# Kernel tuning notes

Hardware: AMD Instinct MI355X
Metric: run time of the kernel (lower is better)

The kernel has to match this reference:

```python
import jax, jax.numpy as jnp
import numpy as np

B, C, H, W = 8, 512, 64, 64
CH = C // 2          # channels per branch after chunk
R = CH // 4          # reduced channels (reduction=4)


def conv1x1(x, w, b):
    # x: [B,c,H,W], w: [o,c], b: [o]  (1x1 conv == per-pixel matmul)
    return jnp.einsum('oc,bchw->bohw', w, x) + b[None, :, None, None]


def spatial_self_corr(x, w1, b1, w2, b2, wo, bo):
    # DANet-style position attention. x: [B,CH,H,W]
    b_, c_, h_, w_ = x.shape
    n = h_ * w_
    q = conv1x1(x, w1, b1).reshape(b_, -1, n)   # [B,R,N]
    k = conv1x1(x, w2, b2).reshape(b_, -1, n)   # [B,R,N]
    attn = jax.nn.softmax(jnp.einsum('brn,brm->bnm', q, k), axis=-1)  # [B,N,N]
    out = jnp.einsum('brn,bnm->brm', k, attn)   # v = k (reduced channels), [B,R,N]
    out = out.reshape(b_, -1, h_, w_)
    return conv1x1(out, wo, bo)                 # [B,CH,H,W]


def channel_self_corr(x, wq, bq, wk, bk, wo, bo):
    # DANet-style channel attention over reduced channels. x: [B,CH,H,W]
    b_, c_, h_, w_ = x.shape
    n = h_ * w_
    q = conv1x1(x, wq, bq).reshape(b_, -1, n)   # [B,R,N]
    k = conv1x1(x, wk, bk).reshape(b_, -1, n)   # [B,R,N]
    attn = jax.nn.softmax(jnp.einsum('brn,bsn->brs', q, k), axis=-1)  # [B,R,R]
    out = jnp.einsum('brs,bsn->brn', attn, k)   # v = k (reduced channels)
    out = out.reshape(b_, -1, h_, w_)
    return conv1x1(out, wo, bo)                 # [B,CH,H,W]


def ckam_forward(top_feat, bottom_feat, wt, bt, wb, bb,
                 s_w1, s_b1, s_w2, s_b2, s_wo, s_bo,
                 c_wq, c_bq, c_wk, c_bk, c_wo, c_bo, f_w, f_b):
    top = conv1x1(top_feat, wt, bt)
    bottom = conv1x1(bottom_feat, wb, bb)
    x = top + bottom                            # [B,C,H,W]
    x1, x2 = jnp.split(x, 2, axis=1)            # each [B,C/2,H,W]
    ssc_out = spatial_self_corr(x1, s_w1, s_b1, s_w2, s_b2, s_wo, s_bo)
    csc_out = channel_self_corr(x2, c_wq, c_bq, c_wk, c_bk, c_wo, c_bo)
    out = jnp.concatenate([ssc_out, csc_out], axis=1)  # [B,C,H,W]
    return conv1x1(out, f_w, f_b)


def setup_inputs() -> dict:
    key = jax.random.key(0)
    ks = jax.random.split(key, 24)
    s = 0.02
    d = {
        'top_feat': jax.random.normal(ks[0], (B, C, H, W), jnp.float32),
        'bottom_feat': jax.random.normal(ks[1], (B, C, H, W), jnp.float32),
        'wt': jax.random.normal(ks[2], (C, C), jnp.float32) * s,
        'bt': jnp.zeros((C,), jnp.float32),
        'wb': jax.random.normal(ks[3], (C, C), jnp.float32) * s,
        'bb': jnp.zeros((C,), jnp.float32),
        's_w1': jax.random.normal(ks[4], (R, CH), jnp.float32) * s,
        's_b1': jnp.zeros((R,), jnp.float32),
        's_w2': jax.random.normal(ks[5], (R, CH), jnp.float32) * s,
        's_b2': jnp.zeros((R,), jnp.float32),
        's_wo': jax.random.normal(ks[6], (CH, R), jnp.float32) * s,
        's_bo': jnp.zeros((CH,), jnp.float32),
        'c_wq': jax.random.normal(ks[7], (R, CH), jnp.float32) * s,
        'c_bq': jnp.zeros((R,), jnp.float32),
        'c_wk': jax.random.normal(ks[8], (R, CH), jnp.float32) * s,
        'c_bk': jnp.zeros((R,), jnp.float32),
        'c_wo': jax.random.normal(ks[9], (CH, R), jnp.float32) * s,
        'c_bo': jnp.zeros((CH,), jnp.float32),
        'f_w': jax.random.normal(ks[10], (C, C), jnp.float32) * s,
        'f_b': jnp.zeros((C,), jnp.float32),
    }
    return d


def reference(top_feat, bottom_feat, wt, bt, wb, bb,
              s_w1, s_b1, s_w2, s_b2, s_wo, s_bo,
              c_wq, c_bq, c_wk, c_bk, c_wo, c_bo, f_w, f_b):
    return ckam_forward(top_feat, bottom_feat, wt, bt, wb, bb,
                        s_w1, s_b1, s_w2, s_b2, s_wo, s_bo,
                        c_wq, c_bq, c_wk, c_bk, c_wo, c_bo, f_w, f_b)
```

## Files before the change

kernel.cpp:

```cpp
#include <hip/hip_runtime.h>

typedef unsigned short u16;
typedef unsigned int   u32;
typedef __attribute__((ext_vector_type(8))) short short8;
typedef __attribute__((ext_vector_type(4))) float f32x4;

__device__ __forceinline__ u16 f2bf(float f) {
  u32 u = __float_as_uint(f);
  u32 r = u + 0x7fffu + ((u >> 16) & 1u);
  return (u16)(r >> 16);
}

__device__ __forceinline__ void gl_lds16(const u16* g, u16* l) {
  __builtin_amdgcn_global_load_lds(
      (const __attribute__((address_space(1))) u32*)g,
      (__attribute__((address_space(3))) u32*)l, 16, 0, 0);
}

__global__ __launch_bounds__(256) void k_combine_qk(
    const float* __restrict__ wt, const float* __restrict__ bt,
    const float* __restrict__ wb, const float* __restrict__ bb,
    const float* __restrict__ s_w1, const float* __restrict__ s_b1,
    const float* __restrict__ s_w2, const float* __restrict__ s_b2,
    const float* __restrict__ c_wq, const float* __restrict__ c_bq,
    const float* __restrict__ c_wk, const float* __restrict__ c_bk,
    u16* __restrict__ Wqkb, float* __restrict__ bqk) {
  int j = blockIdx.x;
  int g = j >> 6, r = j & 63;
  const float* sw; const float* sb;
  if (g == 0)      { sw = s_w1; sb = s_b1; }
  else if (g == 1) { sw = s_w2; sb = s_b2; }
  else if (g == 2) { sw = c_wq; sb = c_bq; }
  else             { sw = c_wk; sb = c_bk; }
  int cbase = (g < 2) ? 0 : 256;

  __shared__ float swr[256];
  __shared__ float red[256];
  int t = threadIdx.x;
  swr[t] = sw[r * 256 + t];
  __syncthreads();

  float a0 = 0.f, a1 = 0.f, a2 = 0.f, a3 = 0.f;
#pragma unroll 4
  for (int c = 0; c < 256; ++c) {
    float a = swr[c];
    int row = (cbase + c) * 512;
    a0 += a * wt[row + t];
    a1 += a * wt[row + 256 + t];
    a2 += a * wb[row + t];
    a3 += a * wb[row + 256 + t];
  }
  Wqkb[j * 1024 + t]       = f2bf(a0);
  Wqkb[j * 1024 + 256 + t] = f2bf(a1);
  Wqkb[j * 1024 + 512 + t] = f2bf(a2);
  Wqkb[j * 1024 + 768 + t] = f2bf(a3);

  red[t] = swr[t] * (bt[cbase + t] + bb[cbase + t]);
  __syncthreads();
  for (int s = 128; s > 0; s >>= 1) {
    if (t < s) red[t] += red[t + s];
    __syncthreads();
  }
  if (t == 0) bqk[j] = red[0] + sb[r];
}

__global__ __launch_bounds__(128) void k_combine_f(
    const float* __restrict__ f_w, const float* __restrict__ f_b,
    const float* __restrict__ s_wo, const float* __restrict__ s_bo,
    const float* __restrict__ c_wo, const float* __restrict__ c_bo,
    u16* __restrict__ Wfb, float* __restrict__ bfb) {
  int o = blockIdx.x;
  int t = threadIdx.x;
  __shared__ float fwr[512];
  __shared__ float red[128];
  for (int i = t; i < 512; i += 128) fwr[i] = f_w[o * 512 + i];
  __syncthreads();

  float acc = 0.f;
  if (t < 64) {
#pragma unroll 4
    for (int c = 0; c < 256; ++c) acc += fwr[c] * s_wo[c * 64 + t];
  } else {
    int rr = t - 64;
#pragma unroll 4
    for (int c = 0; c < 256; ++c) acc += fwr[256 + c] * c_wo[c * 64 + rr];
  }
  Wfb[o * 128 + t] = f2bf(acc);

  red[t] = fwr[t] * s_bo[t] + fwr[t + 128] * s_bo[t + 128]
         + fwr[256 + t] * c_bo[t] + fwr[384 + t] * c_bo[t + 128];
  __syncthreads();
  for (int s = 64; s > 0; s >>= 1) {
    if (t < s) red[t] += red[t + s];
    __syncthreads();
  }
  if (t == 0) bfb[o] = red[0] + f_b[o];
}

__global__ __launch_bounds__(256) void k_gemm_qk_mfma(
    const float* __restrict__ top, const float* __restrict__ bot,
    const u16* __restrict__ Wqkb, const float* __restrict__ bqk,
    float* __restrict__ qk) {
  int b = blockIdx.z, j0 = blockIdx.y * 128, n0 = blockIdx.x * 128;
  __shared__ __align__(16) u16 Aj[2][128][32];
  __shared__ __align__(16) u16 Xs[2][128][32];
  int t = threadIdx.x;
  int wv = t >> 6, lane = t & 63;
  int wr = wv >> 1, wc = wv & 1;
  int q = lane >> 4, l = lane & 15;

  f32x4 acc[4][4];
#pragma unroll
  for (int tr = 0; tr < 4; ++tr)
#pragma unroll
    for (int tc = 0; tc < 4; ++tc) acc[tr][tc] = (f32x4){0.f, 0.f, 0.f, 0.f};

  int xn = t & 31;
  int xs = t >> 5;
  int kx = (xn + (xn >> 2)) & 3;
  int wcol = ((((xs >> 1) ^ kx) << 4) | ((xs & 1) << 3));
  int asr4 = lane >> 2;
  int asc = (lane & 3) ^ ((asr4 + (asr4 >> 2)) & 3);
  int rowA = wr * 64 + l;
  int rowX = wc * 64 + l;
  int fswA = (q ^ ((rowA + (rowA >> 2)) & 3)) << 4;
  int fswX = (q ^ ((rowX + (rowX >> 2)) & 3)) << 4;

  float xva[16], xvb[16];

  auto stageA = [&](int kc, u16* dst) {
#pragma unroll
    for (int pp = 0; pp < 2; ++pp) {
      int p = wv * 2 + pp;
      int row = p * 16 + asr4;
      gl_lds16(Wqkb + (size_t)(j0 + row) * 1024 + kc + asc * 8, dst + p * 512);
    }
  };
  auto loadX = [&](int kc, float (&xv)[16]) {
    const float* src = (kc < 512) ? top : bot;
    int c0 = kc & 511;
    const float* xb = src + (size_t)(b * 512 + c0) * 4096 + n0;
#pragma unroll
    for (int p = 0; p < 4; ++p) {
      int n = xn + 32 * p;
#pragma unroll
      for (int d = 0; d < 4; ++d)
        xv[4 * p + d] = xb[(size_t)(4 * xs + d) * 4096 + n];
    }
  };
  auto writeX = [&](float (&xv)[16], u16* dst) {
    char* base = reinterpret_cast<char*>(dst);
#pragma unroll
    for (int p = 0; p < 4; ++p) {
      int n = xn + 32 * p;
      uint2 pk;
      pk.x = (u32)f2bf(xv[4 * p])     | ((u32)f2bf(xv[4 * p + 1]) << 16);
      pk.y = (u32)f2bf(xv[4 * p + 2]) | ((u32)f2bf(xv[4 * p + 3]) << 16);
      *reinterpret_cast<uint2*>(base + n * 64 + wcol) = pk;
    }
  };
  auto compute = [&](int bufsel) {
    const char* Ab = reinterpret_cast<const char*>(&Aj[bufsel][0][0]);
    const char* Xb = reinterpret_cast<const char*>(&Xs[bufsel][0][0]);
    short8 af[4], bfr[4];
#pragma unroll
    for (int tr = 0; tr < 4; ++tr)
      af[tr] = *reinterpret_cast<const short8*>(Ab + (rowA + tr * 16) * 64 + fswA);
#pragma unroll
    for (int tc = 0; tc < 4; ++tc)
      bfr[tc] = *reinterpret_cast<const short8*>(Xb + (rowX + tc * 16) * 64 + fswX);
#pragma unroll
    for (int tr = 0; tr < 4; ++tr)
#pragma unroll
      for (int tc = 0; tc < 4; ++tc)
        acc[tr][tc] = __builtin_amdgcn_mfma_f32_16x16x32_bf16(
            af[tr], bfr[tc], acc[tr][tc], 0, 0, 0);
  };

  loadX(0, xva);
  stageA(0, &Aj[0][0][0]);
  writeX(xva, &Xs[0][0][0]);
  loadX(32, xvb);
  __syncthreads();

  for (int it2 = 0; it2 < 15; ++it2) {
    int e = it2 * 2;
    loadX((e + 2) * 32, xva);
    stageA((e + 1) * 32, &Aj[1][0][0]);
    writeX(xvb, &Xs[1][0][0]);
    compute(0);
    __syncthreads();
    loadX((e + 3) * 32, xvb);
    stageA((e + 2) * 32, &Aj[0][0][0]);
    writeX(xva, &Xs[0][0][0]);
    compute(1);
    __syncthreads();
  }
  stageA(31 * 32, &Aj[1][0][0]);
  writeX(xvb, &Xs[1][0][0]);
  compute(0);
  __syncthreads();
  compute(1);

#pragma unroll
  for (int tr = 0; tr < 4; ++tr) {
    int j = j0 + wr * 64 + tr * 16 + q * 4;
    float4 bias = *reinterpret_cast<const float4*>(&bqk[j]);
#pragma unroll
    for (int tc = 0; tc < 4; ++tc) {
      int n = n0 + wc * 64 + tc * 16 + l;
      float* dst = qk + (size_t)(b * 256 + j) * 4096 + n;
      dst[0]        = acc[tr][tc][0] + bias.x;
      dst[4096]     = acc[tr][tc][1] + bias.y;
      dst[2 * 4096] = acc[tr][tc][2] + bias.z;
      dst[3 * 4096] = acc[tr][tc][3] + bias.w;
    }
  }
}

__global__ __launch_bounds__(256) void k_transpose_qk(
    const float* __restrict__ qk, u16* __restrict__ q1t, u16* __restrict__ k1t) {
  int b = blockIdx.y, n0 = blockIdx.x * 64;
  __shared__ u16 T[128][68];
  int t = threadIdx.x;
  for (int i = t; i < 8192; i += 256) {
    int j = i >> 6, n = i & 63;
    T[j][n] = f2bf(qk[((size_t)(b * 256) + j) * 4096 + n0 + n]);
  }
  __syncthreads();
  int n = t & 63, h = t >> 6;
  u16 buf[32];
#pragma unroll
  for (int jj = 0; jj < 32; ++jj) buf[jj] = T[h * 32 + jj][n];
  u16* dst;
  if (h < 2) dst = q1t + ((size_t)(b * 4096) + n0 + n) * 64 + h * 32;
  else       dst = k1t + ((size_t)(b * 4096) + n0 + n) * 64 + (h - 2) * 32;
  u32* d32 = reinterpret_cast<u32*>(dst);
#pragma unroll
  for (int k = 0; k < 16; ++k)
    d32[k] = (u32)buf[2 * k] | ((u32)buf[2 * k + 1] << 16);
}

__global__ __launch_bounds__(256) void k_sp_stats_mfma(
    const u16* __restrict__ q1t, const u16* __restrict__ k1t,
    float* __restrict__ dinv) {
  int b = blockIdx.y, n0 = blockIdx.x * 64;
  __shared__ u16 Qs[64][72];
  __shared__ float red[4][64][16];
  int t = threadIdx.x;
  int wv = t >> 6, lane = t & 63;
  int q = lane >> 4, l = lane & 15;

  {
    const u32* src = reinterpret_cast<const u32*>(q1t + ((size_t)(b * 4096) + n0) * 64);
    for (int i = t; i < 2048; i += 256) {
      int n = i >> 5, c = i & 31;
      reinterpret_cast<u32*>(&Qs[n][0])[c] = src[n * 32 + c];
    }
  }
  __syncthreads();

  short8 afr[4][2];
#pragma unroll
  for (int tn = 0; tn < 4; ++tn)
#pragma unroll
    for (int kh = 0; kh < 2; ++kh)
      afr[tn][kh] = *reinterpret_cast<const short8*>(&Qs[tn * 16 + l][kh * 32 + q * 8]);

  const u16* kbase = k1t + (size_t)b * 4096 * 64;
  float dsum[4][4];
#pragma unroll
  for (int tn = 0; tn < 4; ++tn)
#pragma unroll
    for (int i = 0; i < 4; ++i) dsum[tn][i] = 0.f;

  for (int mt = wv; mt < 64; mt += 4) {
    int m0 = mt * 64;
#pragma unroll
    for (int tm = 0; tm < 4; ++tm) {
      const u16* kp = kbase + ((size_t)(m0 + tm * 16 + l)) * 64;
      short8 b0 = *reinterpret_cast<const short8*>(kp + q * 8);
      short8 b1 = *reinterpret_cast<const short8*>(kp + 32 + q * 8);
#pragma unroll
      for (int tn = 0; tn < 4; ++tn) {
        f32x4 acc = {0.f, 0.f, 0.f, 0.f};
        acc = __builtin_amdgcn_mfma_f32_16x16x32_bf16(afr[tn][0], b0, acc, 0, 0, 0);
        acc = __builtin_amdgcn_mfma_f32_16x16x32_bf16(afr[tn][1], b1, acc, 0, 0, 0);
#pragma unroll
        for (int i = 0; i < 4; ++i) dsum[tn][i] += __expf(acc[i]);
      }
    }
  }

#pragma unroll
  for (int tn = 0; tn < 4; ++tn)
#pragma unroll
    for (int i = 0; i < 4; ++i)
      red[wv][tn * 16 + q * 4 + i][l] = dsum[tn][i];
  __syncthreads();
  if (t < 64) {
    float s = 0.f;
#pragma unroll
    for (int v = 0; v < 4; ++v)
#pragma unroll
      for (int u = 0; u < 16; ++u) s += red[v][t][u];
    dinv[(size_t)b * 4096 + n0 + t] = 1.0f / s;
  }
}

__global__ __launch_bounds__(256) void k_scale_k1d(
    const float* __restrict__ qk, const float* __restrict__ dinv,
    u16* __restrict__ k1d) {
  int b = blockIdx.x >> 6, r = blockIdx.x & 63;
  const float* src = qk + ((size_t)(b * 256) + 64 + r) * 4096;
  const float* dv = dinv + (size_t)b * 4096;
  u16* dst = k1d + ((size_t)(b * 64) + r) * 4096;
  for (int i = threadIdx.x; i < 4096; i += 256)
    dst[i] = f2bf(src[i] * dv[i]);
}

#define NSPLIT 2

__device__ __forceinline__ void stage_qk(const u16* qb, const u16* kb, int noff,
                                         u16* qdst, u16* kdst,
                                         int wv, int rsub, int scol) {
#pragma unroll
  for (int pp = 0; pp < 2; ++pp) {
    int p = wv * 2 + pp;
    int row = p * 8 + rsub;
    gl_lds16(qb + ((size_t)(noff + row)) * 64 + scol * 8, qdst + p * 512);
    gl_lds16(kb + (size_t)row * 4096 + noff + scol * 8, kdst + p * 512);
  }
}

__global__ __launch_bounds__(256) void k_sp_apply_mfma(
    const u16* __restrict__ q1t, const u16* __restrict__ k1t,
    const u16* __restrict__ k1d, float* __restrict__ spre) {
  int b = blockIdx.z, m0 = blockIdx.x * 64;
  int n_base = blockIdx.y * (4096 / NSPLIT);
  const int NT = 64 / NSPLIT;

  __shared__ __align__(16) u16 Qs[2][64][64];
  __shared__ __align__(16) u16 Ks[2][64][64];
  __shared__ __align__(16) u16 Wt[64][64];

  int t = threadIdx.x;
  int wv = t >> 6, lane = t & 63;
  int q = lane >> 4, l = lane & 15;
  int sw = l & 7;
  int rsub = lane >> 3;
  int scol = (lane & 7) ^ rsub;

  const u16* ktp = k1t + ((size_t)(b * 4096) + m0 + wv * 16 + l) * 64;
  short8 bS0 = *reinterpret_cast<const short8*>(ktp + q * 8);
  short8 bS1 = *reinterpret_cast<const short8*>(ktp + 32 + q * 8);

  const u16* qb = q1t + (size_t)b * 4096 * 64;
  const u16* kb = k1d + (size_t)b * 64 * 4096;

  f32x4 accO[4];
#pragma unroll
  for (int tr = 0; tr < 4; ++tr) accO[tr] = (f32x4){0.f, 0.f, 0.f, 0.f};

  stage_qk(qb, kb, n_base, &Qs[0][0][0], &Ks[0][0][0], wv, rsub, scol);
  __syncthreads();

  int wrow = wv * 16 + l;
  char* wp = reinterpret_cast<char*>(&Wt[wrow][0]);
  int c_a0 = (q ^ sw) << 4;
  int c_a1 = c_a0 ^ 64;

  int cur = 0;
  for (int nt = 0; nt < NT; ++nt) {
    if (nt + 1 < NT)
      stage_qk(qb, kb, n_base + (nt + 1) * 64,
               &Qs[cur ^ 1][0][0], &Ks[cur ^ 1][0][0], wv, rsub, scol);

    const u16(*Qc)[64] = Qs[cur];
    const u16(*Kc)[64] = Ks[cur];

#pragma unroll
    for (int tn = 0; tn < 4; ++tn) {
      const char* qrow = reinterpret_cast<const char*>(&Qc[tn * 16 + l][0]);
      short8 a0 = *reinterpret_cast<const short8*>(qrow + c_a0);
      short8 a1 = *reinterpret_cast<const short8*>(qrow + c_a1);
      f32x4 s = {0.f, 0.f, 0.f, 0.f};
      s = __builtin_amdgcn_mfma_f32_16x16x32_bf16(a0, bS0, s, 0, 0, 0);
      s = __builtin_amdgcn_mfma_f32_16x16x32_bf16(a1, bS1, s, 0, 0, 0);
      u16 w0 = f2bf(__expf(s[0]));
      u16 w1 = f2bf(__expf(s[1]));
      u16 w2 = f2bf(__expf(s[2]));
      u16 w3 = f2bf(__expf(s[3]));
      uint2 pk;
      pk.x = (u32)w0 | ((u32)w1 << 16);
      pk.y = (u32)w2 | ((u32)w3 << 16);
      *reinterpret_cast<uint2*>(
          wp + ((((tn * 2 + (q >> 1)) ^ sw) << 4) | ((q & 1) << 3))) = pk;
    }

    short8 bW0 = *reinterpret_cast<const short8*>(wp + c_a0);
    short8 bW1 = *reinterpret_cast<const short8*>(wp + c_a1);
#pragma unroll
    for (int tr = 0; tr < 4; ++tr) {
      const char* krow = reinterpret_cast<const char*>(&Kc[tr * 16 + l][0]);
      short8 a0 = *reinterpret_cast<const short8*>(krow + c_a0);
      short8 a1 = *reinterpret_cast<const short8*>(krow + c_a1);
      accO[tr] = __builtin_amdgcn_mfma_f32_16x16x32_bf16(a0, bW0, accO[tr], 0, 0, 0);
      accO[tr] = __builtin_amdgcn_mfma_f32_16x16x32_bf16(a1, bW1, accO[tr], 0, 0, 0);
    }

    __syncthreads();
    cur ^= 1;
  }

#pragma unroll
  for (int tr = 0; tr < 4; ++tr)
#pragma unroll
    for (int i = 0; i < 4; ++i)
      atomicAdd(&spre[(size_t)(b * 64 + tr * 16 + q * 4 + i) * 4096 + m0 + wrow],
                accO[tr][i]);
}

__global__ __launch_bounds__(256) void k_ch_scores(
    const float* __restrict__ qk, float* __restrict__ part) {
  int b = blockIdx.y, ch = blockIdx.x;
  const float* q2 = qk + (size_t)(b * 256 + 128) * 4096;
  const float* k2 = qk + (size_t)(b * 256 + 192) * 4096;
  __shared__ float Qs[64][65];
  __shared__ float Ks[64][65];
  int t = threadIdx.x, ti = t >> 4, tj = t & 15;
  float acc[4][4] = {};

  for (int sub = 0; sub < 2; ++sub) {
    int n0 = ch * 128 + sub * 64;
    __syncthreads();
    for (int i = t; i < 4096; i += 256) {
      int r = i >> 6, n = i & 63;
      Qs[r][n] = q2[(size_t)r * 4096 + n0 + n];
      Ks[r][n] = k2[(size_t)r * 4096 + n0 + n];
    }
    __syncthreads();
#pragma unroll
    for (int n = 0; n < 64; ++n) {
      float qa[4], ka[4];
#pragma unroll
      for (int i = 0; i < 4; ++i) qa[i] = Qs[ti * 4 + i][n];
#pragma unroll
      for (int jx = 0; jx < 4; ++jx) ka[jx] = Ks[tj * 4 + jx][n];
#pragma unroll
      for (int i = 0; i < 4; ++i)
#pragma unroll
        for (int jx = 0; jx < 4; ++jx) acc[i][jx] += qa[i] * ka[jx];
    }
  }
#pragma unroll
  for (int i = 0; i < 4; ++i)
#pragma unroll
    for (int jx = 0; jx < 4; ++jx)
      part[(size_t)(b * 32 + ch) * 4096 + (ti * 4 + i) * 64 + tj * 4 + jx] = acc[i][jx];
}

__global__ __launch_bounds__(64) void k_ch_softmax(
    const float* __restrict__ part, float* __restrict__ attn2) {
  int bid = blockIdx.x;
  int b = bid >> 6, r = bid & 63;
  int s = threadIdx.x;
  const float* p0 = part + (size_t)(b * 32) * 4096 + r * 64 + s;
  float sum = 0.f;
#pragma unroll
  for (int c = 0; c < 32; ++c) sum += p0[(size_t)c * 4096];
  float mx = sum;
#pragma unroll
  for (int o = 32; o > 0; o >>= 1) mx = fmaxf(mx, __shfl_xor(mx, o));
  float e = __expf(sum - mx);
  float den = e;
#pragma unroll
  for (int o = 32; o > 0; o >>= 1) den += __shfl_xor(den, o);
  attn2[(size_t)b * 4096 + r * 64 + s] = e / den;
}

__global__ __launch_bounds__(256) void k_ch_apply(
    const float* __restrict__ qk, const float* __restrict__ attn2,
    float* __restrict__ cpre) {
  int b = blockIdx.y;
  int t = threadIdx.x;
  int n = blockIdx.x * 64 + (t & 63);
  int qr = t >> 6;
  const float* k2 = qk + (size_t)(b * 256 + 192) * 4096;
  __shared__ float As[64][64];
  {
    float4* As4 = reinterpret_cast<float4*>(&As[0][0]);
    const float4* a4 = reinterpret_cast<const float4*>(attn2 + (size_t)b * 4096);
    for (int i = t; i < 1024; i += 256) As4[i] = a4[i];
  }
  __syncthreads();

  float acc[16];
#pragma unroll
  for (int rr = 0; rr < 16; ++rr) acc[rr] = 0.f;
  for (int s4 = 0; s4 < 64; s4 += 4) {
    float kv0 = k2[(size_t)(s4 + 0) * 4096 + n];
    float kv1 = k2[(size_t)(s4 + 1) * 4096 + n];
    float kv2 = k2[(size_t)(s4 + 2) * 4096 + n];
    float kv3 = k2[(size_t)(s4 + 3) * 4096 + n];
#pragma unroll
    for (int rr = 0; rr < 16; ++rr) {
      float4 w = *reinterpret_cast<const float4*>(&As[qr * 16 + rr][s4]);
      acc[rr] += w.x * kv0 + w.y * kv1 + w.z * kv2 + w.w * kv3;
    }
  }
#pragma unroll
  for (int rr = 0; rr < 16; ++rr)
    cpre[(size_t)(b * 64 + qr * 16 + rr) * 4096 + n] = acc[rr];
}

__global__ __launch_bounds__(256) void k_final_mfma(
    const float* __restrict__ spre, const float* __restrict__ cpre,
    const u16* __restrict__ Wfb, const float* __restrict__ bfb,
    float* __restrict__ out) {
  int b = blockIdx.z, o0 = blockIdx.y * 128, n0 = blockIdx.x * 128;
  __shared__ u16 Aj[128][40];
  __shared__ u16 Xs[128][40];
  int t = threadIdx.x;
  int wv = t >> 6, lane = t & 63;
  int wr = wv >> 1, wc = wv & 1;
  int q = lane >> 4, l = lane & 15;

  f32x4 acc[4][4];
#pragma unroll
  for (int tr = 0; tr < 4; ++tr)
#pragma unroll
    for (int tc = 0; tc < 4; ++tc) acc[tr][tc] = (f32x4){0.f, 0.f, 0.f, 0.f};

  int xn = t & 31;
  int xs = t >> 5;

  for (int kc = 0; kc < 128; kc += 32) {
    __syncthreads();
    {
      const u32* asrc = reinterpret_cast<const u32*>(Wfb + (size_t)o0 * 128 + kc);
#pragma unroll
      for (int p = 0; p < 8; ++p) {
        int i = p * 256 + t;
        int row = i >> 4, c = i & 15;
        *reinterpret_cast<u32*>(&Aj[row][c * 2]) = asrc[(size_t)row * 64 + c];
      }
    }
    const float* src = (kc < 64) ? spre : cpre;
    int r0 = (kc < 64) ? kc : kc - 64;
    const float* xb = src + (size_t)(b * 64 + r0) * 4096 + n0;
#pragma unroll
    for (int p = 0; p < 8; ++p) {
      int n = xn + 32 * (p >> 1);
      int kp = xs + 8 * (p & 1);
      float v0 = xb[(size_t)(2 * kp) * 4096 + n];
      float v1 = xb[(size_t)(2 * kp + 1) * 4096 + n];
      *reinterpret_cast<u32*>(&Xs[n][kp * 2]) =
          (u32)f2bf(v0) | ((u32)f2bf(v1) << 16);
    }
    __syncthreads();

    short8 af[4], bfr[4];
#pragma unroll
    for (int tr = 0; tr < 4; ++tr)
      af[tr] = *reinterpret_cast<const short8*>(&Aj[wr * 64 + tr * 16 + l][q * 8]);
#pragma unroll
    for (int tc = 0; tc < 4; ++tc)
      bfr[tc] = *reinterpret_cast<const short8*>(&Xs[wc * 64 + tc * 16 + l][q * 8]);
#pragma unroll
    for (int tr = 0; tr < 4; ++tr)
#pragma unroll
      for (int tc = 0; tc < 4; ++tc)
        acc[tr][tc] = __builtin_amdgcn_mfma_f32_16x16x32_bf16(
            af[tr], bfr[tc], acc[tr][tc], 0, 0, 0);
  }

#pragma unroll
  for (int tr = 0; tr < 4; ++tr) {
    int o = o0 + wr * 64 + tr * 16 + q * 4;
    float4 bias = *reinterpret_cast<const float4*>(&bfb[o]);
#pragma unroll
    for (int tc = 0; tc < 4; ++tc) {
      int n = n0 + wc * 64 + tc * 16 + l;
      float* dst = out + (size_t)(b * 512 + o) * 4096 + n;
      dst[0]        = acc[tr][tc][0] + bias.x;
      dst[4096]     = acc[tr][tc][1] + bias.y;
      dst[2 * 4096] = acc[tr][tc][2] + bias.z;
      dst[3 * 4096] = acc[tr][tc][3] + bias.w;
    }
  }
}

extern "C" void kernel_launch(void* const* d_in, const int* in_sizes, int n_in,
                              void* d_out, int out_size, void* d_ws, size_t ws_size,
                              hipStream_t stream) {
  const float* top  = (const float*)d_in[0];
  const float* bot  = (const float*)d_in[1];
  const float* wt   = (const float*)d_in[2];
  const float* bt   = (const float*)d_in[3];
  const float* wb   = (const float*)d_in[4];
  const float* bb   = (const float*)d_in[5];
  const float* s_w1 = (const float*)d_in[6];
  const float* s_b1 = (const float*)d_in[7];
  const float* s_w2 = (const float*)d_in[8];
  const float* s_b2 = (const float*)d_in[9];
  const float* s_wo = (const float*)d_in[10];
  const float* s_bo = (const float*)d_in[11];
  const float* c_wq = (const float*)d_in[12];
  const float* c_bq = (const float*)d_in[13];
  const float* c_wk = (const float*)d_in[14];
  const float* c_bk = (const float*)d_in[15];
  const float* c_wo = (const float*)d_in[16];
  const float* c_bo = (const float*)d_in[17];
  const float* f_w  = (const float*)d_in[18];
  const float* f_b  = (const float*)d_in[19];
  float* out = (float*)d_out;

  char* ob = (char*)d_out;
  float* qk = (float*)ob;
  u16* q1t = (u16*)(ob + 33554432);
  u16* k1t = (u16*)(ob + 37748736);
  u16* k1d = (u16*)(ob + 41943040);
  float* part = (float*)(ob + 46137344);

  char* ws = (char*)d_ws;
  float* dinv  = (float*)(ws + 0);
  float* attn2 = (float*)(ws + 1179648);
  float* spre  = (float*)(ws + 1310720);
  float* cpre  = (float*)(ws + 9699328);
  u16*   Wqkb  = (u16*)  (ws + 18087936);
  float* bqk   = (float*)(ws + 18612224);
  u16*   Wfb   = (u16*)  (ws + 18613248);
  float* bfb   = (float*)(ws + 18744320);

  hipMemsetAsync(spre, 0, 8388608, stream);

  k_combine_qk<<<256, 256, 0, stream>>>(wt, bt, wb, bb, s_w1, s_b1, s_w2, s_b2,
                                        c_wq, c_bq, c_wk, c_bk, Wqkb, bqk);
  k_combine_f<<<512, 128, 0, stream>>>(f_w, f_b, s_wo, s_bo, c_wo, c_bo, Wfb, bfb);
  k_gemm_qk_mfma<<<dim3(32, 2, 8), 256, 0, stream>>>(top, bot, Wqkb, bqk, qk);
  k_transpose_qk<<<dim3(64, 8), 256, 0, stream>>>(qk, q1t, k1t);
  k_sp_stats_mfma<<<dim3(64, 8), 256, 0, stream>>>(q1t, k1t, dinv);
  k_ch_scores<<<dim3(32, 8), 256, 0, stream>>>(qk, part);
  k_ch_softmax<<<512, 64, 0, stream>>>(part, attn2);
  k_ch_apply<<<dim3(64, 8), 256, 0, stream>>>(qk, attn2, cpre);
  k_scale_k1d<<<512, 256, 0, stream>>>(qk, dinv, k1d);
  k_sp_apply_mfma<<<dim3(64, NSPLIT, 8), 256, 0, stream>>>(q1t, k1t, k1d, spre);
  k_final_mfma<<<dim3(32, 4, 8), 256, 0, stream>>>(spre, cpre, Wfb, bfb, out);
}
```

Before: 436.4 us.

## Shrink QK GEMM tile to 64 rows with swizzled grid and fuse k1d scaling into stats

The QK projection GEMM now uses 64x128 output tiles over a flat 1024-block grid whose block index is remapped so that the four j-tiles sharing an X tile run close together. The aim is more blocks in flight on the many CUs and better L2 reuse of the fp32 input. The cost is that each block reloads and converts X for a smaller slice of outputs. Separately, the row-normaliser scaling of k1 is folded into the softmax-stats kernel, which removes one launch and the dinv round trip through global memory.

```diff
diff --git a/kernel.cpp b/kernel.cpp
--- a/kernel.cpp
+++ b/kernel.cpp
@@ -101,19 +101,24 @@
     const float* __restrict__ top, const float* __restrict__ bot,
     const u16* __restrict__ Wqkb, const float* __restrict__ bqk,
     float* __restrict__ qk) {
-  int b = blockIdx.z, j0 = blockIdx.y * 128, n0 = blockIdx.x * 128;
-  __shared__ __align__(16) u16 Aj[2][128][32];
+  int bid = blockIdx.x;
+  int jt = (bid >> 3) & 3;
+  int idx = (bid >> 5) * 8 + (bid & 7);
+  int j0 = jt * 64;
+  int n0 = (idx & 31) * 128;
+  int b  = idx >> 5;
+
+  __shared__ __align__(16) u16 Aj[2][64][32];
   __shared__ __align__(16) u16 Xs[2][128][32];
   int t = threadIdx.x;
   int wv = t >> 6, lane = t & 63;
-  int wr = wv >> 1, wc = wv & 1;
   int q = lane >> 4, l = lane & 15;
 
-  f32x4 acc[4][4];
+  f32x4 acc[4][2];
 #pragma unroll
   for (int tr = 0; tr < 4; ++tr)
 #pragma unroll
-    for (int tc = 0; tc < 4; ++tc) acc[tr][tc] = (f32x4){0.f, 0.f, 0.f, 0.f};
+    for (int tc = 0; tc < 2; ++tc) acc[tr][tc] = (f32x4){0.f, 0.f, 0.f, 0.f};
 
   int xn = t & 31;
   int xs = t >> 5;
@@ -121,20 +126,13 @@
   int wcol = ((((xs >> 1) ^ kx) << 4) | ((xs & 1) << 3));
   int asr4 = lane >> 2;
   int asc = (lane & 3) ^ ((asr4 + (asr4 >> 2)) & 3);
-  int rowA = wr * 64 + l;
-  int rowX = wc * 64 + l;
-  int fswA = (q ^ ((rowA + (rowA >> 2)) & 3)) << 4;
-  int fswX = (q ^ ((rowX + (rowX >> 2)) & 3)) << 4;
+  int fsw = (q ^ ((l + (l >> 2)) & 3)) << 4;
 
   float xva[16], xvb[16];
 
   auto stageA = [&](int kc, u16* dst) {
-#pragma unroll
-    for (int pp = 0; pp < 2; ++pp) {
-      int p = wv * 2 + pp;
-      int row = p * 16 + asr4;
-      gl_lds16(Wqkb + (size_t)(j0 + row) * 1024 + kc + asc * 8, dst + p * 512);
-    }
+    int row = wv * 16 + asr4;
+    gl_lds16(Wqkb + (size_t)(j0 + row) * 1024 + kc + asc * 8, dst + wv * 512);
   };
   auto loadX = [&](int kc, float (&xv)[16]) {
     const float* src = (kc < 512) ? top : bot;
@@ -162,17 +160,18 @@
   auto compute = [&](int bufsel) {
     const char* Ab = reinterpret_cast<const char*>(&Aj[bufsel][0][0]);
     const char* Xb = reinterpret_cast<const char*>(&Xs[bufsel][0][0]);
-    short8 af[4], bfr[4];
+    short8 af[4], bfr[2];
 #pragma unroll
     for (int tr = 0; tr < 4; ++tr)
-      af[tr] = *reinterpret_cast<const short8*>(Ab + (rowA + tr * 16) * 64 + fswA);
-#pragma unroll
-    for (int tc = 0; tc < 4; ++tc)
-      bfr[tc] = *reinterpret_cast<const short8*>(Xb + (rowX + tc * 16) * 64 + fswX);
+      af[tr] = *reinterpret_cast<const short8*>(Ab + (tr * 16 + l) * 64 + fsw);
+#pragma unroll
+    for (int tc = 0; tc < 2; ++tc)
+      bfr[tc] = *reinterpret_cast<const short8*>(
+          Xb + (wv * 32 + tc * 16 + l) * 64 + fsw);
 #pragma unroll
     for (int tr = 0; tr < 4; ++tr)
 #pragma unroll
-      for (int tc = 0; tc < 4; ++tc)
+      for (int tc = 0; tc < 2; ++tc)
         acc[tr][tc] = __builtin_amdgcn_mfma_f32_16x16x32_bf16(
             af[tr], bfr[tc], acc[tr][tc], 0, 0, 0);
   };
@@ -204,11 +203,11 @@
 
 #pragma unroll
   for (int tr = 0; tr < 4; ++tr) {
-    int j = j0 + wr * 64 + tr * 16 + q * 4;
+    int j = j0 + tr * 16 + q * 4;
     float4 bias = *reinterpret_cast<const float4*>(&bqk[j]);
 #pragma unroll
-    for (int tc = 0; tc < 4; ++tc) {
-      int n = n0 + wc * 64 + tc * 16 + l;
+    for (int tc = 0; tc < 2; ++tc) {
+      int n = n0 + wv * 32 + tc * 16 + l;
       float* dst = qk + (size_t)(b * 256 + j) * 4096 + n;
       dst[0]        = acc[tr][tc][0] + bias.x;
       dst[4096]     = acc[tr][tc][1] + bias.y;
@@ -243,10 +242,11 @@
 
 __global__ __launch_bounds__(256) void k_sp_stats_mfma(
     const u16* __restrict__ q1t, const u16* __restrict__ k1t,
-    float* __restrict__ dinv) {
+    const float* __restrict__ qk, u16* __restrict__ k1d) {
   int b = blockIdx.y, n0 = blockIdx.x * 64;
   __shared__ u16 Qs[64][72];
   __shared__ float red[4][64][16];
+  __shared__ float dvs[64];
   int t = threadIdx.x;
   int wv = t >> 6, lane = t & 63;
   int q = lane >> 4, l = lane & 15;
@@ -304,19 +304,16 @@
     for (int v = 0; v < 4; ++v)
 #pragma unroll
       for (int u = 0; u < 16; ++u) s += red[v][t][u];
-    dinv[(size_t)b * 4096 + n0 + t] = 1.0f / s;
-  }
-}
-
-__global__ __launch_bounds__(256) void k_scale_k1d(
-    const float* __restrict__ qk, const float* __restrict__ dinv,
-    u16* __restrict__ k1d) {
-  int b = blockIdx.x >> 6, r = blockIdx.x & 63;
-  const float* src = qk + ((size_t)(b * 256) + 64 + r) * 4096;
-  const float* dv = dinv + (size_t)b * 4096;
-  u16* dst = k1d + ((size_t)(b * 64) + r) * 4096;
-  for (int i = threadIdx.x; i < 4096; i += 256)
-    dst[i] = f2bf(src[i] * dv[i]);
+    dvs[t] = 1.0f / s;
+  }
+  __syncthreads();
+
+  const float* k1src = qk + ((size_t)(b * 256) + 64) * 4096 + n0;
+  u16* kdst = k1d + (size_t)(b * 64) * 4096 + n0;
+  for (int i = t; i < 4096; i += 256) {
+    int r = i >> 6, n = i & 63;
+    kdst[(size_t)r * 4096 + n] = f2bf(k1src[(size_t)r * 4096 + n] * dvs[n]);
+  }
 }
 
 #define NSPLIT 2
@@ -624,7 +621,6 @@
   float* part = (float*)(ob + 46137344);
 
   char* ws = (char*)d_ws;
-  float* dinv  = (float*)(ws + 0);
   float* attn2 = (float*)(ws + 1179648);
   float* spre  = (float*)(ws + 1310720);
   float* cpre  = (float*)(ws + 9699328);
@@ -638,13 +634,12 @@
   k_combine_qk<<<256, 256, 0, stream>>>(wt, bt, wb, bb, s_w1, s_b1, s_w2, s_b2,
                                         c_wq, c_bq, c_wk, c_bk, Wqkb, bqk);
   k_combine_f<<<512, 128, 0, stream>>>(f_w, f_b, s_wo, s_bo, c_wo, c_bo, Wfb, bfb);
-  k_gemm_qk_mfma<<<dim3(32, 2, 8), 256, 0, stream>>>(top, bot, Wqkb, bqk, qk);
+  k_gemm_qk_mfma<<<1024, 256, 0, stream>>>(top, bot, Wqkb, bqk, qk);
   k_transpose_qk<<<dim3(64, 8), 256, 0, stream>>>(qk, q1t, k1t);
-  k_sp_stats_mfma<<<dim3(64, 8), 256, 0, stream>>>(q1t, k1t, dinv);
+  k_sp_stats_mfma<<<dim3(64, 8), 256, 0, stream>>>(q1t, k1t, qk, k1d);
   k_ch_scores<<<dim3(32, 8), 256, 0, stream>>>(qk, part);
   k_ch_softmax<<<512, 64, 0, stream>>>(part, attn2);
   k_ch_apply<<<dim3(64, 8), 256, 0, stream>>>(qk, attn2, cpre);
-  k_scale_k1d<<<512, 256, 0, stream>>>(qk, dinv, k1d);
   k_sp_apply_mfma<<<dim3(64, NSPLIT, 8), 256, 0, stream>>>(q1t, k1t, k1d, spre);
   k_final_mfma<<<dim3(32, 4, 8), 256, 0, stream>>>(spre, cpre, Wfb, bfb, out);
 }
```

Result: slower. 461.3 us (+5.7%).

## Fuse k1d scaling into spatial stats kernel and relax GEMM barrier waits

Applied to the files above, without the earlier changes.

The per-column softmax denominator is now kept in shared memory, and the stats kernel writes the scaled bf16 K directly. This removes the separate k_scale_k1d launch and the dinv round trip through global memory. Separately, the qk GEMM main loop replaces __syncthreads with explicit s_waitcnt (vmcnt 16, lgkmcnt 0) plus s_barrier, and issues the async A stage before the X loads. The goal is to keep in-flight global loads outstanding across barriers. The hand-tuned vmcnt value is a correctness risk if the count of outstanding loads differs from what is assumed.

```diff
diff --git a/kernel.cpp b/kernel.cpp
--- a/kernel.cpp
+++ b/kernel.cpp
@@ -177,29 +177,33 @@
             af[tr], bfr[tc], acc[tr][tc], 0, 0, 0);
   };
 
+  stageA(0, &Aj[0][0][0]);
   loadX(0, xva);
-  stageA(0, &Aj[0][0][0]);
   writeX(xva, &Xs[0][0][0]);
   loadX(32, xvb);
-  __syncthreads();
+  asm volatile("s_waitcnt lgkmcnt(0)" ::: "memory");
+  __builtin_amdgcn_s_barrier();
 
   for (int it2 = 0; it2 < 15; ++it2) {
     int e = it2 * 2;
+    stageA((e + 1) * 32, &Aj[1][0][0]);
     loadX((e + 2) * 32, xva);
-    stageA((e + 1) * 32, &Aj[1][0][0]);
     writeX(xvb, &Xs[1][0][0]);
     compute(0);
-    __syncthreads();
+    asm volatile("s_waitcnt vmcnt(16) lgkmcnt(0)" ::: "memory");
+    __builtin_amdgcn_s_barrier();
+    stageA((e + 2) * 32, &Aj[0][0][0]);
     loadX((e + 3) * 32, xvb);
-    stageA((e + 2) * 32, &Aj[0][0][0]);
     writeX(xva, &Xs[0][0][0]);
     compute(1);
-    __syncthreads();
+    asm volatile("s_waitcnt vmcnt(16) lgkmcnt(0)" ::: "memory");
+    __builtin_amdgcn_s_barrier();
   }
   stageA(31 * 32, &Aj[1][0][0]);
   writeX(xvb, &Xs[1][0][0]);
   compute(0);
-  __syncthreads();
+  asm volatile("s_waitcnt vmcnt(0) lgkmcnt(0)" ::: "memory");
+  __builtin_amdgcn_s_barrier();
   compute(1);
 
 #pragma unroll
@@ -243,10 +247,11 @@
 
 __global__ __launch_bounds__(256) void k_sp_stats_mfma(
     const u16* __restrict__ q1t, const u16* __restrict__ k1t,
-    float* __restrict__ dinv) {
+    const float* __restrict__ qk, u16* __restrict__ k1d) {
   int b = blockIdx.y, n0 = blockIdx.x * 64;
   __shared__ u16 Qs[64][72];
   __shared__ float red[4][64][16];
+  __shared__ float dvs[64];
   int t = threadIdx.x;
   int wv = t >> 6, lane = t & 63;
   int q = lane >> 4, l = lane & 15;
@@ -304,19 +309,16 @@
     for (int v = 0; v < 4; ++v)
 #pragma unroll
       for (int u = 0; u < 16; ++u) s += red[v][t][u];
-    dinv[(size_t)b * 4096 + n0 + t] = 1.0f / s;
-  }
-}
-
-__global__ __launch_bounds__(256) void k_scale_k1d(
-    const float* __restrict__ qk, const float* __restrict__ dinv,
-    u16* __restrict__ k1d) {
-  int b = blockIdx.x >> 6, r = blockIdx.x & 63;
-  const float* src = qk + ((size_t)(b * 256) + 64 + r) * 4096;
-  const float* dv = dinv + (size_t)b * 4096;
-  u16* dst = k1d + ((size_t)(b * 64) + r) * 4096;
-  for (int i = threadIdx.x; i < 4096; i += 256)
-    dst[i] = f2bf(src[i] * dv[i]);
+    dvs[t] = 1.0f / s;
+  }
+  __syncthreads();
+
+  const float* k1src = qk + ((size_t)(b * 256) + 64) * 4096 + n0;
+  u16* kdst = k1d + (size_t)(b * 64) * 4096 + n0;
+  for (int i = t; i < 4096; i += 256) {
+    int r = i >> 6, n = i & 63;
+    kdst[(size_t)r * 4096 + n] = f2bf(k1src[(size_t)r * 4096 + n] * dvs[n]);
+  }
 }
 
 #define NSPLIT 2
@@ -624,7 +626,6 @@
   float* part = (float*)(ob + 46137344);
 
   char* ws = (char*)d_ws;
-  float* dinv  = (float*)(ws + 0);
   float* attn2 = (float*)(ws + 1179648);
   float* spre  = (float*)(ws + 1310720);
   float* cpre  = (float*)(ws + 9699328);
@@ -640,11 +641,10 @@
   k_combine_f<<<512, 128, 0, stream>>>(f_w, f_b, s_wo, s_bo, c_wo, c_bo, Wfb, bfb);
   k_gemm_qk_mfma<<<dim3(32, 2, 8), 256, 0, stream>>>(top, bot, Wqkb, bqk, qk);
   k_transpose_qk<<<dim3(64, 8), 256, 0, stream>>>(qk, q1t, k1t);
-  k_sp_stats_mfma<<<dim3(64, 8), 256, 0, stream>>>(q1t, k1t, dinv);
+  k_sp_stats_mfma<<<dim3(64, 8), 256, 0, stream>>>(q1t, k1t, qk, k1d);
   k_ch_scores<<<dim3(32, 8), 256, 0, stream>>>(qk, part);
   k_ch_softmax<<<512, 64, 0, stream>>>(part, attn2);
   k_ch_apply<<<dim3(64, 8), 256, 0, stream>>>(qk, attn2, cpre);
-  k_scale_k1d<<<512, 256, 0, stream>>>(qk, dinv, k1d);
   k_sp_apply_mfma<<<dim3(64, NSPLIT, 8), 256, 0, stream>>>(q1t, k1t, k1d, spre);
   k_final_mfma<<<dim3(32, 4, 8), 256, 0, stream>>>(spre, cpre, Wfb, bfb, out);
 }
```

Measured after the change: 433.2 us. No clear change (-0.7%).
